# Performance work log

Hardware: AMD Instinct MI355X
Metric: run time of the kernel (lower is better)

Reference implementation:

```python
import jax, jax.numpy as jnp
import numpy as np

EMBED = 1024
HEADS = 16
HEAD_DIM = EMBED // HEADS


def setup_inputs() -> dict:
    key = jax.random.key(0)
    ks = jax.random.split(key, 8)
    N, S = 4, 2048
    values = jax.random.normal(ks[0], (N, S, EMBED), dtype=jnp.float32)
    keys = jax.random.normal(ks[1], (N, S, EMBED), dtype=jnp.float32)
    query = jax.random.normal(ks[2], (N, S, EMBED), dtype=jnp.float32)
    mask = jnp.ones((N, 1, 1, S), dtype=jnp.int32)
    # per-head shared projections (torch Linear: y = x @ W.T), no bias
    s = 1.0 / np.sqrt(HEAD_DIM)
    Wv = jax.random.uniform(ks[3], (HEAD_DIM, HEAD_DIM), minval=-s, maxval=s, dtype=jnp.float32)
    Wk = jax.random.uniform(ks[4], (HEAD_DIM, HEAD_DIM), minval=-s, maxval=s, dtype=jnp.float32)
    Wq = jax.random.uniform(ks[5], (HEAD_DIM, HEAD_DIM), minval=-s, maxval=s, dtype=jnp.float32)
    so = 1.0 / np.sqrt(EMBED)
    Wo = jax.random.uniform(ks[6], (EMBED, EMBED), minval=-so, maxval=so, dtype=jnp.float32)
    bo = jax.random.uniform(ks[7], (EMBED,), minval=-so, maxval=so, dtype=jnp.float32)
    return {"values": values, "keys": keys, "query": query, "mask": mask,
            "Wv": Wv, "Wk": Wk, "Wq": Wq, "Wo": Wo, "bo": bo}


def reference(values, keys, query, mask, Wv, Wk, Wq, Wo, bo):
    N, S, _ = query.shape
    v = values.reshape(N, -1, HEADS, HEAD_DIM)  # [N,V,H,D]
    k = keys.reshape(N, -1, HEADS, HEAD_DIM)    # [N,K,H,D]
    q = query.reshape(N, -1, HEADS, HEAD_DIM)   # [N,Q,H,D]
    # per-head shared linear projections (x @ W.T)
    v = jnp.einsum('nvhd,ed->nvhe', v, Wv)
    k = jnp.einsum('nkhd,ed->nkhe', k, Wk)
    q = jnp.einsum('nqhd,ed->nqhe', q, Wq)
    energy = jnp.einsum('nqhd,nkhd->nhqk', q, k)  # [N,H,Q,K]
    energy = jnp.where(mask == 0, jnp.float32(-1e20), energy)
    # NOTE: original scales by sqrt(embed_size), not sqrt(head_dim)
    attention = jax.nn.softmax(energy / jnp.float32(np.sqrt(EMBED)), axis=3)
    out = jnp.einsum('nhqk,nkhd->nqhd', attention, v).reshape(N, -1, EMBED)
    return out @ Wo.T + bo
```

## Files before the change

kernel.cpp:

```cpp
#include <hip/hip_runtime.h>
#include <hip/hip_bf16.h>

#define EMBED 1024
#define HEADS 16
#define HDIM 64
#define NB 4
#define SEQ 2048

typedef __bf16 bf16_t;
typedef bf16_t bf16x4 __attribute__((ext_vector_type(4)));
typedef bf16_t bf16x8 __attribute__((ext_vector_type(8)));
typedef float f32x4 __attribute__((ext_vector_type(4)));

static __device__ __forceinline__ bf16x8 cvt8(f32x4 a, f32x4 b) {
    bf16x8 r;
    r[0]=(bf16_t)a[0]; r[1]=(bf16_t)a[1]; r[2]=(bf16_t)a[2]; r[3]=(bf16_t)a[3];
    r[4]=(bf16_t)b[0]; r[5]=(bf16_t)b[1]; r[6]=(bf16_t)b[2]; r[7]=(bf16_t)b[3];
    return r;
}
static __device__ __forceinline__ bf16x8 load_cvt8(const float* __restrict__ p) {
    f32x4 a = *reinterpret_cast<const f32x4*>(p);
    f32x4 b = *reinterpret_cast<const f32x4*>(p + 4);
    return cvt8(a, b);
}
static __device__ __forceinline__ void gload_lds16(const bf16_t* g, bf16_t* l) {
    __builtin_amdgcn_global_load_lds((const __attribute__((address_space(1))) void*)g,
                                     (__attribute__((address_space(3))) void*)l, 16, 0, 0);
}

__global__ __launch_bounds__(256) void qkvproj_kernel(const float* __restrict__ Xq,
                                                      const float* __restrict__ Xk,
                                                      const float* __restrict__ Xv,
                                                      const float* __restrict__ Wq,
                                                      const float* __restrict__ Wk,
                                                      const float* __restrict__ Wv,
                                                      const float* __restrict__ Wo,
                                                      bf16_t* __restrict__ Qo,
                                                      bf16_t* __restrict__ Ko,
                                                      bf16_t* __restrict__ Vo,
                                                      bf16_t* __restrict__ Wob,
                                                      float qscale) {
    const int mode = blockIdx.y;
    if (mode == 3) {
        const size_t i = ((size_t)blockIdx.x * 256 + threadIdx.x) * 8;
        f32x4 a = *reinterpret_cast<const f32x4*>(Wo + i);
        f32x4 b = *reinterpret_cast<const f32x4*>(Wo + i + 4);
        *(bf16x8*)(Wob + i) = cvt8(a, b);
        return;
    }
    const float* X = (mode == 0) ? Xq : (mode == 1) ? Xk : Xv;
    const float* W = (mode == 0) ? Wq : (mode == 1) ? Wk : Wv;
    const int lane = threadIdx.x & 63, w = threadIdx.x >> 6;
    const int lr = lane & 15, g = lane >> 4;
    const int nh = blockIdx.x >> 3;
    const int scb = blockIdx.x & 7;
    const int n = nh >> 4, h = nh & 15;

    bf16x8 wA[4][2];
#pragma unroll
    for (int dt = 0; dt < 4; ++dt) {
        const float* wrow = W + (size_t)(dt * 16 + lr) * HDIM;
        wA[dt][0] = load_cvt8(wrow + g * 8);
        wA[dt][1] = load_cvt8(wrow + 32 + g * 8);
    }

#pragma unroll
    for (int it = 0; it < 4; ++it) {
        const int s0 = scb * 256 + it * 64 + w * 16;
        const float* xrow = X + ((size_t)n * SEQ + s0 + lr) * EMBED + h * HDIM;
        bf16x8 x0 = load_cvt8(xrow + g * 8);
        bf16x8 x1 = load_cvt8(xrow + 32 + g * 8);

        f32x4 acc[4] = {};
#pragma unroll
        for (int dt = 0; dt < 4; ++dt) {
            if (mode == 2) {
                acc[dt] = __builtin_amdgcn_mfma_f32_16x16x32_bf16(x0, wA[dt][0], acc[dt], 0, 0, 0);
                acc[dt] = __builtin_amdgcn_mfma_f32_16x16x32_bf16(x1, wA[dt][1], acc[dt], 0, 0, 0);
            } else {
                acc[dt] = __builtin_amdgcn_mfma_f32_16x16x32_bf16(wA[dt][0], x0, acc[dt], 0, 0, 0);
                acc[dt] = __builtin_amdgcn_mfma_f32_16x16x32_bf16(wA[dt][1], x1, acc[dt], 0, 0, 0);
            }
        }
        if (mode == 2) {
            const int sc4 = scb * 4 + it;
#pragma unroll
            for (int et = 0; et < 4; ++et) {
                bf16x4 o;
#pragma unroll
                for (int r = 0; r < 4; ++r) o[r] = (bf16_t)acc[et][r];
                *(bf16x4*)(Vo + ((size_t)nh * HDIM + et * 16 + lr) * SEQ
                              + sc4 * 64 + ((w >> 1) << 5) + (g << 3) + ((w & 1) << 2)) = o;
            }
        } else {
            bf16_t* Yo = (mode == 0) ? Qo : Ko;
            const float scl = (mode == 0) ? qscale : 1.0f;
#pragma unroll
            for (int dt = 0; dt < 4; ++dt) {
                bf16x4 o;
#pragma unroll
                for (int r = 0; r < 4; ++r) o[r] = (bf16_t)(acc[dt][r] * scl);
                *(bf16x4*)(Yo + ((size_t)nh * SEQ + s0 + lr) * HDIM + dt * 16 + (g << 2)) = o;
            }
        }
    }
}

#define KT 64
#define QPW 32
#define QPB 128
#define NT (SEQ / KT)

__global__ __launch_bounds__(256, 4) void attn_kernel(const bf16_t* __restrict__ Qp,
                                                      const bf16_t* __restrict__ Kp,
                                                      const bf16_t* __restrict__ Vt_g,
                                                      const int* __restrict__ mask,
                                                      bf16_t* __restrict__ AO) {
    __shared__ __align__(16) bf16_t Kt[2][64 * 64];
    __shared__ __align__(16) bf16_t Vt[2][64 * 64];

    const int tid = threadIdx.x;
    const int lane = tid & 63;
    const int w = tid >> 6;
    const int lr = lane & 15, g = lane >> 4;

    const int nh = blockIdx.x & 63;
    const int qb = blockIdx.x >> 6;
    const int n = nh >> 4, h = nh & 15;

    const bf16_t* Qh = Qp + (size_t)nh * SEQ * HDIM;
    const bf16_t* Kh = Kp + (size_t)nh * SEQ * HDIM;
    const bf16_t* Vh = Vt_g + (size_t)nh * HDIM * SEQ;
    const int* mrow = mask + n * SEQ;

    const int q0 = qb * QPB + w * QPW;
    bf16x8 Qreg[2][2];
#pragma unroll
    for (int qt = 0; qt < 2; ++qt)
#pragma unroll
        for (int hf = 0; hf < 2; ++hf)
            Qreg[qt][hf] = *(const bf16x8*)(Qh + (size_t)(q0 + qt * 16 + lr) * HDIM + hf * 32 + g * 8);

    unsigned int mbits = 0;
    for (int t = 0; t < NT; ++t)
        mbits |= (mrow[t * 64 + lane] != 0 ? 1u : 0u) << t;

    const int srow = (w << 3) + (lane >> 3);
    const int sx = (lane & 7) ^ (srow & 7);

#define STAGE(t, b) { \
    gload_lds16(Kh + ((size_t)((t) * 64 + srow)) * 64 + sx * 8,      &Kt[b][0]    + w * 512); \
    gload_lds16(Kh + ((size_t)((t) * 64 + srow + 32)) * 64 + sx * 8, &Kt[b][2048] + w * 512); \
    gload_lds16(Vh + (size_t)srow * SEQ + (t) * 64 + sx * 8,         &Vt[b][0]    + w * 512); \
    gload_lds16(Vh + (size_t)(srow + 32) * SEQ + (t) * 64 + sx * 8,  &Vt[b][2048] + w * 512); }

    f32x4 accO[2][4] = {};
    f32x4 accL[2] = {};
    bf16x8 ones;
#pragma unroll
    for (int j = 0; j < 8; ++j) ones[j] = (bf16_t)1.0f;

    STAGE(0, 0);

    for (int t = 0; t < NT; ++t) {
        const int cur = t & 1;
        asm volatile("s_waitcnt vmcnt(0)" ::: "memory");
        __builtin_amdgcn_s_barrier();
        __builtin_amdgcn_sched_barrier(0);
        if (t + 1 < NT) STAGE(t + 1, cur ^ 1);

        const bf16_t* Kb = &Kt[cur][0];
        const bf16_t* Vb = &Vt[cur][0];

        const int mbit = (int)((mbits >> t) & 1u);
        const bool allone = __all(mbit);

        unsigned int pwl[2][4], pwh[2][4];
#pragma unroll
        for (int ct = 0; ct < 4; ++ct) {
            int row = ct * 16 + lr, rs = row & 7;
            bf16x8 kf0 = *(const bf16x8*)(Kb + row * 64 + ((g ^ rs) << 3));
            bf16x8 kf1 = *(const bf16x8*)(Kb + row * 64 + (((4 + g) ^ rs) << 3));
#pragma unroll
            for (int qt = 0; qt < 2; ++qt) {
                f32x4 z = {};
                z = __builtin_amdgcn_mfma_f32_16x16x32_bf16(kf0, Qreg[qt][0], z, 0, 0, 0);
                z = __builtin_amdgcn_mfma_f32_16x16x32_bf16(kf1, Qreg[qt][1], z, 0, 0, 0);
                if (allone) {
#pragma unroll
                    for (int r = 0; r < 4; ++r) z[r] = __builtin_amdgcn_exp2f(z[r]);
                } else {
#pragma unroll
                    for (int r = 0; r < 4; ++r) {
                        int key = ct * 16 + g * 4 + r;
                        int mk = __shfl(mbit, key);
                        z[r] = mk ? __builtin_amdgcn_exp2f(z[r]) : 0.f;
                    }
                }
                unsigned int w0, w1;
                asm("v_cvt_pk_bf16_f32 %0, %1, %2" : "=v"(w0) : "v"(z[0]), "v"(z[1]));
                asm("v_cvt_pk_bf16_f32 %0, %1, %2" : "=v"(w1) : "v"(z[2]), "v"(z[3]));
                if (ct == 0)      { pwl[qt][0] = w0; pwl[qt][1] = w1; }
                else if (ct == 1) { pwl[qt][2] = w0; pwl[qt][3] = w1; }
                else if (ct == 2) { pwh[qt][0] = w0; pwh[qt][1] = w1; }
                else              { pwh[qt][2] = w0; pwh[qt][3] = w1; }
            }
        }

        __builtin_amdgcn_s_setprio(1);
#pragma unroll
        for (int qt = 0; qt < 2; ++qt) {
            bf16x8 pa0 = *(const bf16x8*)&pwl[qt][0];
            bf16x8 pa1 = *(const bf16x8*)&pwh[qt][0];
            accL[qt] = __builtin_amdgcn_mfma_f32_16x16x32_bf16(pa0, ones, accL[qt], 0, 0, 0);
            accL[qt] = __builtin_amdgcn_mfma_f32_16x16x32_bf16(pa1, ones, accL[qt], 0, 0, 0);
        }
#pragma unroll
        for (int ctd = 0; ctd < 4; ++ctd) {
            int row = ctd * 16 + lr, rs = row & 7;
            bf16x8 vf0 = *(const bf16x8*)(Vb + row * 64 + ((g ^ rs) << 3));
            bf16x8 vf1 = *(const bf16x8*)(Vb + row * 64 + (((4 + g) ^ rs) << 3));
#pragma unroll
            for (int qt = 0; qt < 2; ++qt) {
                bf16x8 pa0 = *(const bf16x8*)&pwl[qt][0];
                bf16x8 pa1 = *(const bf16x8*)&pwh[qt][0];
                accO[qt][ctd] = __builtin_amdgcn_mfma_f32_16x16x32_bf16(pa0, vf0, accO[qt][ctd], 0, 0, 0);
                accO[qt][ctd] = __builtin_amdgcn_mfma_f32_16x16x32_bf16(pa1, vf1, accO[qt][ctd], 0, 0, 0);
            }
        }
        __builtin_amdgcn_s_setprio(0);
    }
#undef STAGE

#pragma unroll
    for (int qt = 0; qt < 2; ++qt)
#pragma unroll
        for (int r = 0; r < 4; ++r) {
            float inv = 1.0f / accL[qt][r];
            int q = q0 + qt * 16 + g * 4 + r;
            bf16_t* orow = AO + ((size_t)(n * SEQ + q)) * EMBED + h * HDIM;
#pragma unroll
            for (int ctd = 0; ctd < 4; ++ctd)
                orow[ctd * 16 + lr] = (bf16_t)(accO[qt][ctd][r] * inv);
        }
}

__global__ __launch_bounds__(256, 2) void outproj_kernel(const bf16_t* __restrict__ Xa,
                                                         const bf16_t* __restrict__ Wob,
                                                         const float* __restrict__ bo,
                                                         float* __restrict__ Out) {
    __shared__ __align__(16) bf16_t As[2][128 * 64];
    __shared__ __align__(16) bf16_t Bs[2][128 * 64];
    const int tid = threadIdx.x;
    const int lane = tid & 63, w = tid >> 6;
    const int lr = lane & 15, g = lane >> 4;
    const int wm = w >> 1, wn = w & 1;
    const int bm = blockIdx.x & 63;
    const int bn = blockIdx.x >> 6;
    const int r0 = bm * 128, c0 = bn * 128;

    int srow[4], scx[4];
#pragma unroll
    for (int p = 0; p < 4; ++p) {
        srow[p] = p * 32 + w * 8 + (lane >> 3);
        scx[p] = (lane & 7) ^ (srow[p] & 7);
    }

#define STG(s, b) { _Pragma("unroll") for (int p = 0; p < 4; ++p) { \
    gload_lds16(Xa  + (size_t)(r0 + srow[p]) * EMBED + (s) * 64 + scx[p] * 8, &As[b][0] + (p * 256 + w * 64) * 8); \
    gload_lds16(Wob + (size_t)(c0 + srow[p]) * EMBED + (s) * 64 + scx[p] * 8, &Bs[b][0] + (p * 256 + w * 64) * 8); } }

    f32x4 acc[4][4] = {};

    STG(0, 0);

    for (int ks = 0; ks < 16; ++ks) {
        const int cur = ks & 1;
        asm volatile("s_waitcnt vmcnt(0)" ::: "memory");
        __builtin_amdgcn_s_barrier();
        __builtin_amdgcn_sched_barrier(0);
        if (ks + 1 < 16) STG(ks + 1, cur ^ 1);

        const bf16_t* Ab = As[cur];
        const bf16_t* Bb = Bs[cur];
#pragma unroll
        for (int hf = 0; hf < 2; ++hf) {
            bf16x8 af[4], bfr[4];
#pragma unroll
            for (int i = 0; i < 4; ++i) {
                int ar = wm * 64 + i * 16 + lr;
                af[i] = *(const bf16x8*)(Ab + ar * 64 + (((hf * 4 + g) ^ (ar & 7)) << 3));
                int br = wn * 64 + i * 16 + lr;
                bfr[i] = *(const bf16x8*)(Bb + br * 64 + (((hf * 4 + g) ^ (br & 7)) << 3));
            }
            __builtin_amdgcn_s_setprio(1);
#pragma unroll
            for (int i = 0; i < 4; ++i)
#pragma unroll
                for (int j = 0; j < 4; ++j)
                    acc[i][j] = __builtin_amdgcn_mfma_f32_16x16x32_bf16(af[i], bfr[j], acc[i][j], 0, 0, 0);
            __builtin_amdgcn_s_setprio(0);
        }
    }
#undef STG

#pragma unroll
    for (int i = 0; i < 4; ++i)
#pragma unroll
        for (int r = 0; r < 4; ++r) {
            int row = r0 + wm * 64 + i * 16 + g * 4 + r;
            float* orow = Out + (size_t)row * EMBED;
#pragma unroll
            for (int j = 0; j < 4; ++j) {
                int col = c0 + wn * 64 + j * 16 + lr;
                orow[col] = acc[i][j][r] + bo[col];
            }
        }
}

extern "C" void kernel_launch(void* const* d_in, const int* in_sizes, int n_in,
                              void* d_out, int out_size, void* d_ws, size_t ws_size,
                              hipStream_t stream) {
    const float* values = (const float*)d_in[0];
    const float* keys   = (const float*)d_in[1];
    const float* query  = (const float*)d_in[2];
    const int*   mask   = (const int*)d_in[3];
    const float* Wv = (const float*)d_in[4];
    const float* Wk = (const float*)d_in[5];
    const float* Wq = (const float*)d_in[6];
    const float* Wo = (const float*)d_in[7];
    const float* bo = (const float*)d_in[8];
    float* out = (float*)d_out;

    char* ws = (char*)d_ws;
    const size_t SZ = (size_t)NB * HEADS * SEQ * HDIM * sizeof(bf16_t);
    bf16_t* Qp  = (bf16_t*)(ws);
    bf16_t* Kp  = (bf16_t*)(ws + SZ);
    bf16_t* Vt  = (bf16_t*)(ws + 2 * SZ);
    bf16_t* Xa  = (bf16_t*)(ws + 3 * SZ);
    bf16_t* Wob = (bf16_t*)(ws + 4 * SZ);

    const float qscale = 0.0450842200278f;

    dim3 blk(256);
    dim3 gproj(512, 4);
    qkvproj_kernel<<<gproj, blk, 0, stream>>>(query, keys, values, Wq, Wk, Wv, Wo,
                                              Qp, Kp, Vt, Wob, qscale);

    const int attn_grid = 64 * (SEQ / QPB);
    attn_kernel<<<dim3(attn_grid), blk, 0, stream>>>(Qp, Kp, Vt, mask, Xa);

    outproj_kernel<<<dim3(512), blk, 0, stream>>>(Xa, Wob, bo, out);
}
```

Before: 141.1 us.

## Store Q and K in FP8 and use FP8 MFMA for QK^T

Measured after the change: 129.8 us. 8.0% less time.

```diff
diff --git a/kernel.cpp b/kernel.cpp
--- a/kernel.cpp
+++ b/kernel.cpp
@@ -11,6 +11,7 @@
 typedef bf16_t bf16x4 __attribute__((ext_vector_type(4)));
 typedef bf16_t bf16x8 __attribute__((ext_vector_type(8)));
 typedef float f32x4 __attribute__((ext_vector_type(4)));
+typedef unsigned char u8;
 
 static __device__ __forceinline__ bf16x8 cvt8(f32x4 a, f32x4 b) {
     bf16x8 r;
@@ -26,6 +27,15 @@
 static __device__ __forceinline__ void gload_lds16(const bf16_t* g, bf16_t* l) {
     __builtin_amdgcn_global_load_lds((const __attribute__((address_space(1))) void*)g,
                                      (__attribute__((address_space(3))) void*)l, 16, 0, 0);
+}
+static __device__ __forceinline__ void gload_lds16u(const u8* g, u8* l) {
+    __builtin_amdgcn_global_load_lds((const __attribute__((address_space(1))) void*)g,
+                                     (__attribute__((address_space(3))) void*)l, 16, 0, 0);
+}
+static __device__ __forceinline__ unsigned int pk_fp8x4(float z0, float z1, float z2, float z3) {
+    unsigned int ww = __builtin_amdgcn_cvt_pk_fp8_f32(z0, z1, 0, false);
+    ww = __builtin_amdgcn_cvt_pk_fp8_f32(z2, z3, ww, true);
+    return ww;
 }
 
 __global__ __launch_bounds__(256) void qkvproj_kernel(const float* __restrict__ Xq,
@@ -35,11 +45,10 @@
                                                       const float* __restrict__ Wk,
                                                       const float* __restrict__ Wv,
                                                       const float* __restrict__ Wo,
-                                                      bf16_t* __restrict__ Qo,
-                                                      bf16_t* __restrict__ Ko,
+                                                      u8* __restrict__ Qo,
+                                                      u8* __restrict__ Ko,
                                                       bf16_t* __restrict__ Vo,
-                                                      bf16_t* __restrict__ Wob,
-                                                      float qscale) {
+                                                      bf16_t* __restrict__ Wob) {
     const int mode = blockIdx.y;
     if (mode == 3) {
         const size_t i = ((size_t)blockIdx.x * 256 + threadIdx.x) * 8;
@@ -93,14 +102,11 @@
                               + sc4 * 64 + ((w >> 1) << 5) + (g << 3) + ((w & 1) << 2)) = o;
             }
         } else {
-            bf16_t* Yo = (mode == 0) ? Qo : Ko;
-            const float scl = (mode == 0) ? qscale : 1.0f;
+            u8* Yo = (mode == 0) ? Qo : Ko;
 #pragma unroll
             for (int dt = 0; dt < 4; ++dt) {
-                bf16x4 o;
-#pragma unroll
-                for (int r = 0; r < 4; ++r) o[r] = (bf16_t)(acc[dt][r] * scl);
-                *(bf16x4*)(Yo + ((size_t)nh * SEQ + s0 + lr) * HDIM + dt * 16 + (g << 2)) = o;
+                unsigned int ww = pk_fp8x4(acc[dt][0], acc[dt][1], acc[dt][2], acc[dt][3]);
+                *(unsigned int*)(Yo + ((size_t)nh * SEQ + s0 + lr) * HDIM + dt * 16 + (g << 2)) = ww;
             }
         }
     }
@@ -110,13 +116,14 @@
 #define QPW 32
 #define QPB 128
 #define NT (SEQ / KT)
-
-__global__ __launch_bounds__(256, 4) void attn_kernel(const bf16_t* __restrict__ Qp,
-                                                      const bf16_t* __restrict__ Kp,
+#define KOFF(row, cc) ((row) * 64 + (((((cc) >> 1) ^ (((row) >> 1) & 3)) << 4) | (((cc) & 1) << 3)))
+
+__global__ __launch_bounds__(256, 4) void attn_kernel(const u8* __restrict__ Qp,
+                                                      const u8* __restrict__ Kp,
                                                       const bf16_t* __restrict__ Vt_g,
                                                       const int* __restrict__ mask,
                                                       bf16_t* __restrict__ AO) {
-    __shared__ __align__(16) bf16_t Kt[2][64 * 64];
+    __shared__ __align__(16) u8 Kt[2][4096];
     __shared__ __align__(16) bf16_t Vt[2][64 * 64];
 
     const int tid = threadIdx.x;
@@ -128,31 +135,34 @@
     const int qb = blockIdx.x >> 6;
     const int n = nh >> 4, h = nh & 15;
 
-    const bf16_t* Qh = Qp + (size_t)nh * SEQ * HDIM;
-    const bf16_t* Kh = Kp + (size_t)nh * SEQ * HDIM;
+    const u8* Qh = Qp + (size_t)nh * SEQ * HDIM;
+    const u8* Kh = Kp + (size_t)nh * SEQ * HDIM;
     const bf16_t* Vh = Vt_g + (size_t)nh * HDIM * SEQ;
     const int* mrow = mask + n * SEQ;
 
+    const float qscale = 0.0450842200278f;
+
     const int q0 = qb * QPB + w * QPW;
-    bf16x8 Qreg[2][2];
+    long Qreg[2][2];
 #pragma unroll
     for (int qt = 0; qt < 2; ++qt)
 #pragma unroll
-        for (int hf = 0; hf < 2; ++hf)
-            Qreg[qt][hf] = *(const bf16x8*)(Qh + (size_t)(q0 + qt * 16 + lr) * HDIM + hf * 32 + g * 8);
+        for (int kh = 0; kh < 2; ++kh)
+            Qreg[qt][kh] = *(const long*)(Qh + (size_t)(q0 + qt * 16 + lr) * HDIM + kh * 32 + g * 8);
 
     unsigned int mbits = 0;
     for (int t = 0; t < NT; ++t)
         mbits |= (mrow[t * 64 + lane] != 0 ? 1u : 0u) << t;
 
+    const int grow = tid >> 2;
+    const int glog = (tid & 3) ^ ((grow >> 1) & 3);
     const int srow = (w << 3) + (lane >> 3);
     const int sx = (lane & 7) ^ (srow & 7);
 
 #define STAGE(t, b) { \
-    gload_lds16(Kh + ((size_t)((t) * 64 + srow)) * 64 + sx * 8,      &Kt[b][0]    + w * 512); \
-    gload_lds16(Kh + ((size_t)((t) * 64 + srow + 32)) * 64 + sx * 8, &Kt[b][2048] + w * 512); \
-    gload_lds16(Vh + (size_t)srow * SEQ + (t) * 64 + sx * 8,         &Vt[b][0]    + w * 512); \
-    gload_lds16(Vh + (size_t)(srow + 32) * SEQ + (t) * 64 + sx * 8,  &Vt[b][2048] + w * 512); }
+    gload_lds16u(Kh + ((size_t)((t) * 64 + grow)) * 64 + glog * 16, &Kt[b][0] + tid * 16); \
+    gload_lds16(Vh + (size_t)srow * SEQ + (t) * 64 + sx * 8,        &Vt[b][0]    + w * 512); \
+    gload_lds16(Vh + (size_t)(srow + 32) * SEQ + (t) * 64 + sx * 8, &Vt[b][2048] + w * 512); }
 
     f32x4 accO[2][4] = {};
     f32x4 accL[2] = {};
@@ -169,7 +179,7 @@
         __builtin_amdgcn_sched_barrier(0);
         if (t + 1 < NT) STAGE(t + 1, cur ^ 1);
 
-        const bf16_t* Kb = &Kt[cur][0];
+        const u8* Kb = &Kt[cur][0];
         const bf16_t* Vb = &Vt[cur][0];
 
         const int mbit = (int)((mbits >> t) & 1u);
@@ -178,23 +188,23 @@
         unsigned int pwl[2][4], pwh[2][4];
 #pragma unroll
         for (int ct = 0; ct < 4; ++ct) {
-            int row = ct * 16 + lr, rs = row & 7;
-            bf16x8 kf0 = *(const bf16x8*)(Kb + row * 64 + ((g ^ rs) << 3));
-            bf16x8 kf1 = *(const bf16x8*)(Kb + row * 64 + (((4 + g) ^ rs) << 3));
+            int row = ct * 16 + lr;
+            long kf0 = *(const long*)(Kb + KOFF(row, g));
+            long kf1 = *(const long*)(Kb + KOFF(row, 4 + g));
 #pragma unroll
             for (int qt = 0; qt < 2; ++qt) {
                 f32x4 z = {};
-                z = __builtin_amdgcn_mfma_f32_16x16x32_bf16(kf0, Qreg[qt][0], z, 0, 0, 0);
-                z = __builtin_amdgcn_mfma_f32_16x16x32_bf16(kf1, Qreg[qt][1], z, 0, 0, 0);
+                z = __builtin_amdgcn_mfma_f32_16x16x32_fp8_fp8(kf0, Qreg[qt][0], z, 0, 0, 0);
+                z = __builtin_amdgcn_mfma_f32_16x16x32_fp8_fp8(kf1, Qreg[qt][1], z, 0, 0, 0);
                 if (allone) {
 #pragma unroll
-                    for (int r = 0; r < 4; ++r) z[r] = __builtin_amdgcn_exp2f(z[r]);
+                    for (int r = 0; r < 4; ++r) z[r] = __builtin_amdgcn_exp2f(z[r] * qscale);
                 } else {
 #pragma unroll
                     for (int r = 0; r < 4; ++r) {
                         int key = ct * 16 + g * 4 + r;
                         int mk = __shfl(mbit, key);
-                        z[r] = mk ? __builtin_amdgcn_exp2f(z[r]) : 0.f;
+                        z[r] = mk ? __builtin_amdgcn_exp2f(z[r] * qscale) : 0.f;
                     }
                 }
                 unsigned int w0, w1;
@@ -333,19 +343,18 @@
     float* out = (float*)d_out;
 
     char* ws = (char*)d_ws;
-    const size_t SZ = (size_t)NB * HEADS * SEQ * HDIM * sizeof(bf16_t);
-    bf16_t* Qp  = (bf16_t*)(ws);
-    bf16_t* Kp  = (bf16_t*)(ws + SZ);
-    bf16_t* Vt  = (bf16_t*)(ws + 2 * SZ);
-    bf16_t* Xa  = (bf16_t*)(ws + 3 * SZ);
-    bf16_t* Wob = (bf16_t*)(ws + 4 * SZ);
-
-    const float qscale = 0.0450842200278f;
+    const size_t SZ8  = (size_t)NB * HEADS * SEQ * HDIM;
+    const size_t SZBF = SZ8 * sizeof(bf16_t);
+    u8* Qp      = (u8*)(ws);
+    u8* Kp      = (u8*)(ws + SZ8);
+    bf16_t* Vt  = (bf16_t*)(ws + 2 * SZ8);
+    bf16_t* Xa  = (bf16_t*)(ws + 2 * SZ8 + SZBF);
+    bf16_t* Wob = (bf16_t*)(ws + 2 * SZ8 + 2 * SZBF);
 
     dim3 blk(256);
     dim3 gproj(512, 4);
     qkvproj_kernel<<<gproj, blk, 0, stream>>>(query, keys, values, Wq, Wk, Wv, Wo,
-                                              Qp, Kp, Vt, Wob, qscale);
+                                              Qp, Kp, Vt, Wob);
 
     const int attn_grid = 64 * (SEQ / QPB);
     attn_kernel<<<dim3(attn_grid), blk, 0, stream>>>(Qp, Kp, Vt, mask, Xa);
```
